# Performance work log

Hardware: AMD Instinct MI355X
Metric: run time of the kernel (lower is better)

## Reference

```python
import jax, jax.numpy as jnp
import numpy as np


def setup_inputs() -> dict:
    B, Lq, Lk, D, F, H = 2, 2048, 2048, 128, 128, 8
    key = jax.random.key(0)
    ks = jax.random.split(key, 8)
    X_Q = jax.random.normal(ks[0], (B, Lq, D), dtype=jnp.float32)
    X_K = jax.random.normal(ks[1], (B, Lk, D), dtype=jnp.float32)
    X_V = jax.random.normal(ks[2], (B, Lk, F), dtype=jnp.float32)
    mask = jax.random.randint(ks[3], (B, 1, Lq, Lk), 0, 2, dtype=jnp.int32)
    # xavier_normal for [H, D, D]: std = sqrt(2/(D+D))
    W_Q = jax.random.normal(ks[4], (H, D, D), dtype=jnp.float32) * np.sqrt(2.0 / (D + D))
    W_K = jax.random.normal(ks[5], (H, D, D), dtype=jnp.float32) * np.sqrt(2.0 / (D + D))
    W_V = jax.random.normal(ks[6], (H, F, F), dtype=jnp.float32) * np.sqrt(2.0 / (F + F))
    O = jax.random.normal(ks[7], (F * H, F), dtype=jnp.float32) * np.sqrt(2.0 / (F * H + F))
    return {"X_Q": X_Q, "X_K": X_K, "X_V": X_V, "mask": mask,
            "W_Q": W_Q, "W_K": W_K, "W_V": W_V, "O": O}


def reference(X_Q, X_K, X_V, mask, W_Q, W_K, W_V, O):
    B, Lq, D = X_Q.shape
    H = W_Q.shape[0]
    F = W_V.shape[1]
    # torch.einsum with repeated in-operand index ('hdd') takes the diagonal
    dq = jnp.diagonal(W_Q, axis1=1, axis2=2)  # [H, D]
    dk = jnp.diagonal(W_K, axis1=1, axis2=2)  # [H, D]
    dv = jnp.diagonal(W_V, axis1=1, axis2=2)  # [H, F]
    g = dq * dk                               # fused per-head QK diagonal scale [H, D]
    scale = 1.0 / jnp.sqrt(jnp.asarray(D, dtype=X_Q.dtype))
    scores = jnp.einsum('bqd,hd,bkd->bhqk', X_Q, g, X_K) * scale  # [B,H,Lq,Lk]
    scores = jnp.where(mask == 0, jnp.asarray(-jnp.inf, scores.dtype), scores)
    A = jax.nn.softmax(scores, axis=-1)
    # O_h = A @ (diag(dv_h) scaled V)
    Oh = jnp.einsum('bhqk,hf,bkf->bhqf', A, dv, X_V)  # [B,H,Lq,F]
    Oh = Oh.transpose(0, 2, 1, 3).reshape(B, Lq, H * F)
    return jnp.einsum('bqx,xf->bqf', Oh, O)
```

## Files before the change

kernel.cpp:

```cpp
#include <hip/hip_runtime.h>

typedef __bf16 bf16;
typedef __bf16 bf16x4 __attribute__((ext_vector_type(4)));
typedef __bf16 bf16x8 __attribute__((ext_vector_type(8)));
typedef float f32x4 __attribute__((ext_vector_type(4)));
typedef short s16x4 __attribute__((ext_vector_type(4)));
typedef unsigned int u32;
typedef unsigned long long u64;

#define B_ 2
#define H_ 8
#define L_ 2048
#define D_ 128
#define F_ 128
#define QT 128
#define KT 64
#define NKT (L_ / KT)

#define WS_KB 0u
#define WS_VT (1u << 20)
#define WS_MB (2u << 20)

#define SMEM_BYTES 102400
#define POX_STRIDE 132
#define SOH_OFF 67584
#define SOH_STRIDE 136
#define SO2_STRIDE 136

__device__ __forceinline__ void dma16(const void* g, void* l) {
    __builtin_amdgcn_global_load_lds(
        (const __attribute__((address_space(1))) u32*)g,
        (__attribute__((address_space(3))) u32*)l, 16, 0, 0);
}

__device__ __forceinline__ f32x4 mfma32(bf16x8 a, bf16x8 b, f32x4 c) {
    return __builtin_amdgcn_mfma_f32_16x16x32_bf16(a, b, c, 0, 0, 0);
}

__device__ __forceinline__ f32x4 mfma16(bf16x4 a, bf16x4 b, f32x4 c) {
#if __has_builtin(__builtin_amdgcn_mfma_f32_16x16x16_bf16)
    return __builtin_amdgcn_mfma_f32_16x16x16_bf16(a, b, c, 0, 0, 0);
#else
    s16x4 as = __builtin_bit_cast(s16x4, a);
    s16x4 bs = __builtin_bit_cast(s16x4, b);
    return __builtin_amdgcn_mfma_f32_16x16x16bf16_1k(as, bs, c, 0, 0, 0);
#endif
}

__device__ __forceinline__ float fexp2(float x) {
#if __has_builtin(__builtin_amdgcn_exp2f)
    return __builtin_amdgcn_exp2f(x);
#else
    return __builtin_exp2f(x);
#endif
}

__global__ __launch_bounds__(256)
void prep_all(const float* __restrict__ XK, const float* __restrict__ XV,
              const int* __restrict__ mask, bf16* __restrict__ Kb,
              bf16* __restrict__ Vtb, u64* __restrict__ bits)
{
    const int bid = blockIdx.x;
    const int tid = threadIdx.x;
    if (bid < 8192) {
        int wv = bid * 4 + (tid >> 6);
        int lane = tid & 63;
        size_t base = (size_t)wv * 256;
        #pragma unroll
        for (int s = 0; s < 4; ++s) {
            int m = mask[base + s * 64 + lane];
            u64 bal = __ballot(m != 0);
            if (lane == 0) bits[(size_t)wv * 4 + s] = bal;
        }
    } else if (bid < 8448) {
        int gid = (bid - 8192) * 256 + tid;
        int row = gid >> 4;
        int j   = gid & 15;
        const float* src = XK + (size_t)row * 128 + j * 8;
        float4 v0 = *(const float4*)src;
        float4 v1 = *(const float4*)(src + 4);
        bf16x8 w;
        w[0] = (bf16)v0.x; w[1] = (bf16)v0.y; w[2] = (bf16)v0.z; w[3] = (bf16)v0.w;
        w[4] = (bf16)v1.x; w[5] = (bf16)v1.y; w[6] = (bf16)v1.z; w[7] = (bf16)v1.w;
        int jp = j ^ (row & 15);
        *(bf16x8*)(Kb + (size_t)row * 128 + jp * 8) = w;
    } else {
        int idx  = bid - 8448;
        int tile = idx >> 2;
        int fq   = idx & 3;
        int f    = fq * 32 + (tid & 31);
        int j    = tid >> 5;
        int bb   = tile >> 5, kt = tile & 31;
        const float* src = XV + ((size_t)(bb * L_ + kt * 64 + j * 8)) * F_ + f;
        bf16x4 w0, w1;
        #pragma unroll
        for (int jj = 0; jj < 4; ++jj) {
            w0[jj] = (bf16)src[(size_t)jj * F_];
            w1[jj] = (bf16)src[(size_t)(4 + jj) * F_];
        }
        bf16* outp = Vtb + (size_t)tile * 8192 + f * 64;
        *(bf16x4*)(outp + (((2 * j) ^ (f & 15)) * 4)) = w0;
        *(bf16x4*)(outp + (((2 * j + 1) ^ (f & 15)) * 4)) = w1;
    }
}

__global__ __launch_bounds__(512, 2)
void attn_fused_kernel(const float* __restrict__ XQ, const bf16* __restrict__ Kb,
                       const bf16* __restrict__ Vtb, const u64* __restrict__ bits,
                       const float* __restrict__ WQ, const float* __restrict__ WK,
                       const float* __restrict__ WV, const float* __restrict__ Om,
                       float* __restrict__ out)
{
    __shared__ __align__(16) char smem[SMEM_BYTES];
    __shared__ __align__(16) float g_s[128];
    __shared__ __align__(16) float lws[256];

    bf16* sK0 = (bf16*)smem;
    bf16* sK1 = (bf16*)(smem + 16384);
    bf16* sV0 = (bf16*)(smem + 32768);
    bf16* sV1 = (bf16*)(smem + 49152);
    float* pOx = (float*)smem;
    bf16* sOh  = (bf16*)(smem + SOH_OFF);
    bf16* sO2t = (bf16*)smem;

    const int tid  = threadIdx.x;
    const int wave = tid >> 6;
    const int lane = tid & 63;
    const int c    = lane & 15;
    const int quad = lane >> 4;
    const int qt = blockIdx.x, h = blockIdx.y, b = blockIdx.z;
    const int q0 = qt * QT;

    const int kh   = wave >> 2;
    const int msel = wave & 3;
    const int fv  = tid & 127;
    const int grp = tid >> 7;

    if (tid < 128) {
        float wq = WQ[(h * D_ + tid) * D_ + tid];
        float wk = WK[(h * D_ + tid) * D_ + tid];
        g_s[tid] = wq * wk * 0.08838834764831845f * 1.4426950408889634f;
    }
    __syncthreads();

    const char* gKbase = (const char*)Kb + (size_t)(b * L_) * 256;
    const char* gVbase = (const char*)Vtb + (size_t)(b * NKT) * 16384;

    #pragma unroll
    for (int i = 0; i < 2; ++i) dma16(gKbase + i * 8192 + tid * 16, (char*)sK0 + i * 8192 + tid * 16);
    #pragma unroll
    for (int i = 0; i < 2; ++i) dma16(gVbase + i * 8192 + tid * 16, (char*)sV0 + i * 8192 + tid * 16);

    bf16x8 qfrag[2][4];
    #pragma unroll
    for (int qs = 0; qs < 2; ++qs) {
        const float* qrow = XQ + (size_t)(b * L_ + q0 + (qs * 4 + msel) * 16 + c) * D_;
        #pragma unroll
        for (int kc = 0; kc < 4; ++kc) {
            int d0 = kc * 32 + quad * 8;
            float4 v0 = *(const float4*)(qrow + d0);
            float4 v1 = *(const float4*)(qrow + d0 + 4);
            float4 g0 = *(const float4*)(g_s + d0);
            float4 g1 = *(const float4*)(g_s + d0 + 4);
            bf16x8 w;
            w[0] = (bf16)(v0.x * g0.x); w[1] = (bf16)(v0.y * g0.y);
            w[2] = (bf16)(v0.z * g0.z); w[3] = (bf16)(v0.w * g0.w);
            w[4] = (bf16)(v1.x * g1.x); w[5] = (bf16)(v1.y * g1.y);
            w[6] = (bf16)(v1.z * g1.z); w[7] = (bf16)(v1.w * g1.w);
            qfrag[qs][kc] = w;
        }
    }

    f32x4 oacc[2][8];
    #pragma unroll
    for (int qs = 0; qs < 2; ++qs)
        #pragma unroll
        for (int fi = 0; fi < 8; ++fi)
            #pragma unroll
            for (int r = 0; r < 4; ++r) oacc[qs][fi][r] = 0.f;
    float lsum0 = 0.f, lsum1 = 0.f;

    const u64* mrowA = bits + (size_t)(b * L_ + q0 + msel * 16 + c) * NKT;
    const u64* mrowB = bits + (size_t)(b * L_ + q0 + (msel + 4) * 16 + c) * NKT;

    #pragma unroll 2
    for (int kt = 0; kt < NKT; ++kt) {
        bf16* sK  = (kt & 1) ? sK1 : sK0;
        bf16* sV  = (kt & 1) ? sV1 : sV0;
        bf16* sKn = (kt & 1) ? sK0 : sK1;
        bf16* sVn = (kt & 1) ? sV0 : sV1;

        asm volatile("s_barrier" ::: "memory");

        u64 mb0 = mrowA[kt];
        u64 mb1 = mrowB[kt];

        if (kt + 1 < NKT) {
            const char* gk = gKbase + (size_t)(kt + 1) * 16384;
            const char* gv = gVbase + (size_t)(kt + 1) * 16384;
            #pragma unroll
            for (int i = 0; i < 2; ++i) dma16(gk + i * 8192 + tid * 16, (char*)sKn + i * 8192 + tid * 16);
            #pragma unroll
            for (int i = 0; i < 2; ++i) dma16(gv + i * 8192 + tid * 16, (char*)sVn + i * 8192 + tid * 16);
            asm volatile("s_waitcnt vmcnt(6)" ::: "memory");
        } else {
            asm volatile("s_waitcnt vmcnt(2)" ::: "memory");
        }
        asm volatile("s_barrier" ::: "memory");

        f32x4 tacc[2][2];
        #pragma unroll
        for (int qs = 0; qs < 2; ++qs)
            #pragma unroll
            for (int kti = 0; kti < 2; ++kti)
                #pragma unroll
                for (int r = 0; r < 4; ++r) tacc[qs][kti][r] = 0.f;

        #pragma unroll
        for (int kti = 0; kti < 2; ++kti) {
            const bf16* krow = sK + ((kh * 2 + kti) * 16 + c) * 128;
            #pragma unroll
            for (int kc = 0; kc < 4; ++kc) {
                bf16x8 kfrag = *(const bf16x8*)(krow + (((kc * 4 + quad) ^ c) * 8));
                tacc[0][kti] = mfma32(kfrag, qfrag[0][kc], tacc[0][kti]);
                tacc[1][kti] = mfma32(kfrag, qfrag[1][kc], tacc[1][kti]);
            }
        }

        bf16x4 pfrag[2][2];
        #pragma unroll
        for (int kti = 0; kti < 2; ++kti) {
            #pragma unroll
            for (int r = 0; r < 4; ++r) {
                int bit = kh * 32 + kti * 16 + quad * 4 + r;
                float p0 = ((mb0 >> bit) & 1ull) ? fexp2(tacc[0][kti][r]) : 0.f;
                float p1 = ((mb1 >> bit) & 1ull) ? fexp2(tacc[1][kti][r]) : 0.f;
                lsum0 += p0; lsum1 += p1;
                pfrag[0][kti][r] = (bf16)p0;
                pfrag[1][kti][r] = (bf16)p1;
            }
        }

        #pragma unroll
        for (int fi = 0; fi < 8; ++fi) {
            #pragma unroll
            for (int kti = 0; kti < 2; ++kti) {
                int g = kh * 8 + kti * 4 + quad;
                bf16x4 vfrag = *(const bf16x4*)(sV + (fi * 16 + c) * 64 + ((g ^ c) * 4));
                oacc[0][fi] = mfma16(pfrag[0][kti], vfrag, oacc[0][fi]);
                oacc[1][fi] = mfma16(pfrag[1][kti], vfrag, oacc[1][fi]);
            }
        }
    }

    {
        float v0 = lsum0;
        v0 += __shfl_xor(v0, 16); v0 += __shfl_xor(v0, 32);
        if (lane < 16) lws[kh * 128 + msel * 16 + lane] = v0;
        float v1 = lsum1;
        v1 += __shfl_xor(v1, 16); v1 += __shfl_xor(v1, 32);
        if (lane < 16) lws[kh * 128 + (msel + 4) * 16 + lane] = v1;
    }
    if (tid < 128)
        g_s[tid] = WV[(h * F_ + tid) * F_ + tid];
    __syncthreads();

    if (kh == 1) {
        #pragma unroll
        for (int qs = 0; qs < 2; ++qs)
            #pragma unroll
            for (int fi = 0; fi < 8; ++fi)
                #pragma unroll
                for (int r = 0; r < 4; ++r)
                    pOx[((qs * 4 + msel) * 16 + quad * 4 + r) * POX_STRIDE + fi * 16 + c] = oacc[qs][fi][r];
    }
    __syncthreads();

    if (kh == 0) {
        #pragma unroll
        for (int qs = 0; qs < 2; ++qs) {
            int mt = qs * 4 + msel;
            float linv[4];
            #pragma unroll
            for (int r = 0; r < 4; ++r) {
                int m16 = quad * 4 + r;
                linv[r] = 1.0f / (lws[mt * 16 + m16] + lws[128 + mt * 16 + m16]);
            }
            #pragma unroll
            for (int fi = 0; fi < 8; ++fi)
                #pragma unroll
                for (int r = 0; r < 4; ++r) {
                    int row = mt * 16 + quad * 4 + r;
                    float v = (oacc[qs][fi][r] + pOx[row * POX_STRIDE + fi * 16 + c]) * linv[r];
                    sOh[row * SOH_STRIDE + fi * 16 + c] = (bf16)v;
                }
        }
    }
    __syncthreads();

    #pragma unroll
    for (int i = 0; i < 8; ++i) {
        int fp4 = grp * 32 + i * 4;
        bf16x4 w;
        #pragma unroll
        for (int j = 0; j < 4; ++j) {
            int x = fp4 + j;
            w[j] = (bf16)(Om[(h * F_ + x) * F_ + fv] * g_s[x]);
        }
        *(bf16x4*)(sO2t + fv * SO2_STRIDE + fp4) = w;
    }
    __syncthreads();

    const int pm = wave;
    bf16x8 afr[4];
    const bf16* ohrow = sOh + (pm * 16 + c) * SOH_STRIDE;
    #pragma unroll
    for (int kc = 0; kc < 4; ++kc)
        afr[kc] = *(const bf16x8*)(ohrow + kc * 32 + quad * 8);

    #pragma unroll
    for (int nt = 0; nt < 8; ++nt) {
        f32x4 pacc;
        #pragma unroll
        for (int r = 0; r < 4; ++r) pacc[r] = 0.f;
        const bf16* orow = sO2t + (nt * 16 + c) * SO2_STRIDE;
        #pragma unroll
        for (int kc = 0; kc < 4; ++kc) {
            bf16x8 bfrag = *(const bf16x8*)(orow + kc * 32 + quad * 8);
            pacc = mfma32(afr[kc], bfrag, pacc);
        }
        #pragma unroll
        for (int r = 0; r < 4; ++r) {
            int qg = q0 + pm * 16 + quad * 4 + r;
            atomicAdd(out + ((size_t)(b * L_ + qg) * F_ + nt * 16 + c), pacc[r]);
        }
    }
}

extern "C" void kernel_launch(void* const* d_in, const int* in_sizes, int n_in,
                              void* d_out, int out_size, void* d_ws, size_t ws_size,
                              hipStream_t stream) {
    const float* XQ   = (const float*)d_in[0];
    const float* XK   = (const float*)d_in[1];
    const float* XV   = (const float*)d_in[2];
    const int*   mask = (const int*)d_in[3];
    const float* WQ   = (const float*)d_in[4];
    const float* WK   = (const float*)d_in[5];
    const float* WV   = (const float*)d_in[6];
    const float* Om   = (const float*)d_in[7];
    float* out = (float*)d_out;

    char* ws = (char*)d_ws;
    bf16* Kb   = (bf16*)(ws + WS_KB);
    bf16* Vtb  = (bf16*)(ws + WS_VT);
    u64*  bits = (u64*)(ws + WS_MB);

    prep_all<<<8704, 256, 0, stream>>>(XK, XV, mask, Kb, Vtb, bits);
    hipMemsetAsync(out, 0, (size_t)out_size * sizeof(float), stream);

    dim3 grid(L_ / QT, H_, B_);
    attn_fused_kernel<<<grid, 512, 0, stream>>>(XQ, Kb, Vtb, bits, WQ, WK, WV, Om, out);
}
```

Measured before the change: 170.5 us.

## Halve query tile, split keys across four wave groups, raise occupancy

Shrinks the query tile from 128 to 64 rows and splits each 64-key tile across four wave groups instead of two, so each wave does half the score/PV work per tile. Shared memory drops and launch bounds request 4 blocks per CU, doubling the grid and aiming for more resident waves to hide latency. The mask word for the next tile is prefetched alongside the DMA, and the cross-wave output reduction now runs in two swizzled passes over three partial buffers. In exchange, each block reloads the full K/V stream for half as many queries, doubling K/V traffic, and the epilogue needs more barriers and reduction work.

```diff
diff --git a/kernel.cpp b/kernel.cpp
--- a/kernel.cpp
+++ b/kernel.cpp
@@ -13,7 +13,7 @@
 #define L_ 2048
 #define D_ 128
 #define F_ 128
-#define QT 128
+#define QT 64
 #define KT 64
 #define NKT (L_ / KT)
 
@@ -21,9 +21,8 @@
 #define WS_VT (1u << 20)
 #define WS_MB (2u << 20)
 
-#define SMEM_BYTES 102400
-#define POX_STRIDE 132
-#define SOH_OFF 67584
+#define SMEM_BYTES 66560
+#define SOH_OFF 49152
 #define SOH_STRIDE 136
 #define SO2_STRIDE 136
 
@@ -104,7 +103,7 @@
     }
 }
 
-__global__ __launch_bounds__(512, 2)
+__global__ __launch_bounds__(512, 4)
 void attn_fused_kernel(const float* __restrict__ XQ, const bf16* __restrict__ Kb,
                        const bf16* __restrict__ Vtb, const u64* __restrict__ bits,
                        const float* __restrict__ WQ, const float* __restrict__ WK,
@@ -131,8 +130,8 @@
     const int qt = blockIdx.x, h = blockIdx.y, b = blockIdx.z;
     const int q0 = qt * QT;
 
-    const int kh   = wave >> 2;
-    const int msel = wave & 3;
+    const int kq = wave >> 1;
+    const int mp = wave & 1;
     const int fv  = tid & 127;
     const int grp = tid >> 7;
 
@@ -151,10 +150,15 @@
     #pragma unroll
     for (int i = 0; i < 2; ++i) dma16(gVbase + i * 8192 + tid * 16, (char*)sV0 + i * 8192 + tid * 16);
 
+    const u64* mrowA = bits + (size_t)(b * L_ + q0 + mp * 16 + c) * NKT;
+    const u64* mrowB = bits + (size_t)(b * L_ + q0 + (mp + 2) * 16 + c) * NKT;
+    u64 mb0c = mrowA[0];
+    u64 mb1c = mrowB[0];
+
     bf16x8 qfrag[2][4];
     #pragma unroll
     for (int qs = 0; qs < 2; ++qs) {
-        const float* qrow = XQ + (size_t)(b * L_ + q0 + (qs * 4 + msel) * 16 + c) * D_;
+        const float* qrow = XQ + (size_t)(b * L_ + q0 + (qs * 2 + mp) * 16 + c) * D_;
         #pragma unroll
         for (int kc = 0; kc < 4; ++kc) {
             int d0 = kc * 32 + quad * 8;
@@ -180,9 +184,6 @@
             for (int r = 0; r < 4; ++r) oacc[qs][fi][r] = 0.f;
     float lsum0 = 0.f, lsum1 = 0.f;
 
-    const u64* mrowA = bits + (size_t)(b * L_ + q0 + msel * 16 + c) * NKT;
-    const u64* mrowB = bits + (size_t)(b * L_ + q0 + (msel + 4) * 16 + c) * NKT;
-
     #pragma unroll 2
     for (int kt = 0; kt < NKT; ++kt) {
         bf16* sK  = (kt & 1) ? sK1 : sK0;
@@ -192,8 +193,8 @@
 
         asm volatile("s_barrier" ::: "memory");
 
-        u64 mb0 = mrowA[kt];
-        u64 mb1 = mrowB[kt];
+        u64 mb0 = mb0c;
+        u64 mb1 = mb1c;
 
         if (kt + 1 < NKT) {
             const char* gk = gKbase + (size_t)(kt + 1) * 16384;
@@ -202,53 +203,48 @@
             for (int i = 0; i < 2; ++i) dma16(gk + i * 8192 + tid * 16, (char*)sKn + i * 8192 + tid * 16);
             #pragma unroll
             for (int i = 0; i < 2; ++i) dma16(gv + i * 8192 + tid * 16, (char*)sVn + i * 8192 + tid * 16);
+            mb0c = mrowA[kt + 1];
+            mb1c = mrowB[kt + 1];
             asm volatile("s_waitcnt vmcnt(6)" ::: "memory");
         } else {
             asm volatile("s_waitcnt vmcnt(2)" ::: "memory");
         }
         asm volatile("s_barrier" ::: "memory");
 
-        f32x4 tacc[2][2];
+        f32x4 tacc[2];
         #pragma unroll
         for (int qs = 0; qs < 2; ++qs)
             #pragma unroll
-            for (int kti = 0; kti < 2; ++kti)
-                #pragma unroll
-                for (int r = 0; r < 4; ++r) tacc[qs][kti][r] = 0.f;
-
-        #pragma unroll
-        for (int kti = 0; kti < 2; ++kti) {
-            const bf16* krow = sK + ((kh * 2 + kti) * 16 + c) * 128;
+            for (int r = 0; r < 4; ++r) tacc[qs][r] = 0.f;
+
+        {
+            const bf16* krow = sK + (kq * 16 + c) * 128;
             #pragma unroll
             for (int kc = 0; kc < 4; ++kc) {
                 bf16x8 kfrag = *(const bf16x8*)(krow + (((kc * 4 + quad) ^ c) * 8));
-                tacc[0][kti] = mfma32(kfrag, qfrag[0][kc], tacc[0][kti]);
-                tacc[1][kti] = mfma32(kfrag, qfrag[1][kc], tacc[1][kti]);
+                tacc[0] = mfma32(kfrag, qfrag[0][kc], tacc[0]);
+                tacc[1] = mfma32(kfrag, qfrag[1][kc], tacc[1]);
             }
         }
 
-        bf16x4 pfrag[2][2];
-        #pragma unroll
-        for (int kti = 0; kti < 2; ++kti) {
-            #pragma unroll
-            for (int r = 0; r < 4; ++r) {
-                int bit = kh * 32 + kti * 16 + quad * 4 + r;
-                float p0 = ((mb0 >> bit) & 1ull) ? fexp2(tacc[0][kti][r]) : 0.f;
-                float p1 = ((mb1 >> bit) & 1ull) ? fexp2(tacc[1][kti][r]) : 0.f;
-                lsum0 += p0; lsum1 += p1;
-                pfrag[0][kti][r] = (bf16)p0;
-                pfrag[1][kti][r] = (bf16)p1;
-            }
-        }
-
-        #pragma unroll
-        for (int fi = 0; fi < 8; ++fi) {
-            #pragma unroll
-            for (int kti = 0; kti < 2; ++kti) {
-                int g = kh * 8 + kti * 4 + quad;
+        bf16x4 pfrag[2];
+        #pragma unroll
+        for (int r = 0; r < 4; ++r) {
+            int bit = kq * 16 + quad * 4 + r;
+            float p0 = ((mb0 >> bit) & 1ull) ? fexp2(tacc[0][r]) : 0.f;
+            float p1 = ((mb1 >> bit) & 1ull) ? fexp2(tacc[1][r]) : 0.f;
+            lsum0 += p0; lsum1 += p1;
+            pfrag[0][r] = (bf16)p0;
+            pfrag[1][r] = (bf16)p1;
+        }
+
+        {
+            int g = kq * 4 + quad;
+            #pragma unroll
+            for (int fi = 0; fi < 8; ++fi) {
                 bf16x4 vfrag = *(const bf16x4*)(sV + (fi * 16 + c) * 64 + ((g ^ c) * 4));
-                oacc[0][fi] = mfma16(pfrag[0][kti], vfrag, oacc[0][fi]);
-                oacc[1][fi] = mfma16(pfrag[1][kti], vfrag, oacc[1][fi]);
+                oacc[0][fi] = mfma16(pfrag[0], vfrag, oacc[0][fi]);
+                oacc[1][fi] = mfma16(pfrag[1], vfrag, oacc[1][fi]);
             }
         }
     }
@@ -256,47 +252,60 @@
     {
         float v0 = lsum0;
         v0 += __shfl_xor(v0, 16); v0 += __shfl_xor(v0, 32);
-        if (lane < 16) lws[kh * 128 + msel * 16 + lane] = v0;
+        if (lane < 16) lws[kq * 64 + mp * 16 + lane] = v0;
         float v1 = lsum1;
         v1 += __shfl_xor(v1, 16); v1 += __shfl_xor(v1, 32);
-        if (lane < 16) lws[kh * 128 + (msel + 4) * 16 + lane] = v1;
+        if (lane < 16) lws[kq * 64 + (mp + 2) * 16 + lane] = v1;
     }
     if (tid < 128)
         g_s[tid] = WV[(h * F_ + tid) * F_ + tid];
     __syncthreads();
 
-    if (kh == 1) {
+    float linv[2][4];
+    if (kq == 0) {
         #pragma unroll
         for (int qs = 0; qs < 2; ++qs)
             #pragma unroll
-            for (int fi = 0; fi < 8; ++fi)
+            for (int r = 0; r < 4; ++r) {
+                int row = (qs * 2 + mp) * 16 + quad * 4 + r;
+                linv[qs][r] = 1.0f /
+                    (lws[row] + lws[64 + row] + lws[128 + row] + lws[192 + row]);
+            }
+    }
+
+    #pragma unroll
+    for (int r2 = 0; r2 < 2; ++r2) {
+        if (kq != 0) {
+            float* dst = pOx + (kq - 1) * 4096;
+            #pragma unroll
+            for (int qs = 0; qs < 2; ++qs)
                 #pragma unroll
-                for (int r = 0; r < 4; ++r)
-                    pOx[((qs * 4 + msel) * 16 + quad * 4 + r) * POX_STRIDE + fi * 16 + c] = oacc[qs][fi][r];
-    }
-    __syncthreads();
-
-    if (kh == 0) {
-        #pragma unroll
-        for (int qs = 0; qs < 2; ++qs) {
-            int mt = qs * 4 + msel;
-            float linv[4];
-            #pragma unroll
-            for (int r = 0; r < 4; ++r) {
-                int m16 = quad * 4 + r;
-                linv[r] = 1.0f / (lws[mt * 16 + m16] + lws[128 + mt * 16 + m16]);
-            }
-            #pragma unroll
-            for (int fi = 0; fi < 8; ++fi)
+                for (int fl = 0; fl < 4; ++fl)
+                    #pragma unroll
+                    for (int r = 0; r < 4; ++r) {
+                        int row = (qs * 2 + mp) * 16 + quad * 4 + r;
+                        int col = (fl * 16 + c) ^ (quad << 4);
+                        dst[row * 64 + col] = oacc[qs][r2 * 4 + fl][r];
+                    }
+        }
+        __syncthreads();
+        if (kq == 0) {
+            #pragma unroll
+            for (int qs = 0; qs < 2; ++qs)
                 #pragma unroll
-                for (int r = 0; r < 4; ++r) {
-                    int row = mt * 16 + quad * 4 + r;
-                    float v = (oacc[qs][fi][r] + pOx[row * POX_STRIDE + fi * 16 + c]) * linv[r];
-                    sOh[row * SOH_STRIDE + fi * 16 + c] = (bf16)v;
-                }
-        }
-    }
-    __syncthreads();
+                for (int fl = 0; fl < 4; ++fl)
+                    #pragma unroll
+                    for (int r = 0; r < 4; ++r) {
+                        int fi = r2 * 4 + fl;
+                        int row = (qs * 2 + mp) * 16 + quad * 4 + r;
+                        int col = (fl * 16 + c) ^ (quad << 4);
+                        float v = oacc[qs][fi][r] + pOx[row * 64 + col]
+                                + pOx[4096 + row * 64 + col] + pOx[8192 + row * 64 + col];
+                        sOh[row * SOH_STRIDE + fi * 16 + c] = (bf16)(v * linv[qs][r]);
+                    }
+        }
+        __syncthreads();
+    }
 
     #pragma unroll
     for (int i = 0; i < 8; ++i) {
@@ -311,7 +320,8 @@
     }
     __syncthreads();
 
-    const int pm = wave;
+    const int pm = wave & 3;
+    const int pf = wave >> 2;
     bf16x8 afr[4];
     const bf16* ohrow = sOh + (pm * 16 + c) * SOH_STRIDE;
     #pragma unroll
@@ -319,11 +329,11 @@
         afr[kc] = *(const bf16x8*)(ohrow + kc * 32 + quad * 8);
 
     #pragma unroll
-    for (int nt = 0; nt < 8; ++nt) {
+    for (int nt = 0; nt < 4; ++nt) {
         f32x4 pacc;
         #pragma unroll
         for (int r = 0; r < 4; ++r) pacc[r] = 0.f;
-        const bf16* orow = sO2t + (nt * 16 + c) * SO2_STRIDE;
+        const bf16* orow = sO2t + ((pf * 4 + nt) * 16 + c) * SO2_STRIDE;
         #pragma unroll
         for (int kc = 0; kc < 4; ++kc) {
             bf16x8 bfrag = *(const bf16x8*)(orow + kc * 32 + quad * 8);
@@ -332,7 +342,7 @@
         #pragma unroll
         for (int r = 0; r < 4; ++r) {
             int qg = q0 + pm * 16 + quad * 4 + r;
-            atomicAdd(out + ((size_t)(b * L_ + qg) * F_ + nt * 16 + c), pacc[r]);
+            atomicAdd(out + ((size_t)(b * L_ + qg) * F_ + (pf * 4 + nt) * 16 + c), pacc[r]);
         }
     }
 }
```

New measurement: 527.9 us. 3.1x slower.

## Halve query tile to 64 rows, doubling grid and cutting LDS and registers

Applied to the files above, without the earlier changes.

The query tile shrinks from 128 to 64 rows, so each wave handles one 16-row M-tile instead of two. This halves accumulator registers and LDS use, and the grid doubles to 512 blocks, which should improve occupancy and load balance across CUs. The change also prefetches mask words one iteration ahead with adjusted waitcnt, raises wave priority during the MFMA section, and splits the output projection across waves by N. In exchange, each K/V tile is reused by half as many queries, so global K/V traffic per output doubles.

```diff
diff --git a/kernel.cpp b/kernel.cpp
--- a/kernel.cpp
+++ b/kernel.cpp
@@ -13,7 +13,7 @@
 #define L_ 2048
 #define D_ 128
 #define F_ 128
-#define QT 128
+#define QT 64
 #define KT 64
 #define NKT (L_ / KT)
 
@@ -21,9 +21,10 @@
 #define WS_VT (1u << 20)
 #define WS_MB (2u << 20)
 
-#define SMEM_BYTES 102400
+#define SMEM_BYTES 66048
+#define LWS_OFF 65536
 #define POX_STRIDE 132
-#define SOH_OFF 67584
+#define SOH_OFF 36864
 #define SOH_STRIDE 136
 #define SO2_STRIDE 136
 
@@ -104,7 +105,7 @@
     }
 }
 
-__global__ __launch_bounds__(512, 2)
+__global__ __launch_bounds__(512)
 void attn_fused_kernel(const float* __restrict__ XQ, const bf16* __restrict__ Kb,
                        const bf16* __restrict__ Vtb, const u64* __restrict__ bits,
                        const float* __restrict__ WQ, const float* __restrict__ WK,
@@ -113,12 +114,12 @@
 {
     __shared__ __align__(16) char smem[SMEM_BYTES];
     __shared__ __align__(16) float g_s[128];
-    __shared__ __align__(16) float lws[256];
 
     bf16* sK0 = (bf16*)smem;
     bf16* sK1 = (bf16*)(smem + 16384);
     bf16* sV0 = (bf16*)(smem + 32768);
     bf16* sV1 = (bf16*)(smem + 49152);
+    float* lws = (float*)(smem + LWS_OFF);
     float* pOx = (float*)smem;
     bf16* sOh  = (bf16*)(smem + SOH_OFF);
     bf16* sO2t = (bf16*)smem;
@@ -151,10 +152,12 @@
     #pragma unroll
     for (int i = 0; i < 2; ++i) dma16(gVbase + i * 8192 + tid * 16, (char*)sV0 + i * 8192 + tid * 16);
 
-    bf16x8 qfrag[2][4];
-    #pragma unroll
-    for (int qs = 0; qs < 2; ++qs) {
-        const float* qrow = XQ + (size_t)(b * L_ + q0 + (qs * 4 + msel) * 16 + c) * D_;
+    const u64* mrow = bits + (size_t)(b * L_ + q0 + msel * 16 + c) * NKT;
+    u64 mbc = mrow[0];
+
+    bf16x8 qfrag[4];
+    {
+        const float* qrow = XQ + (size_t)(b * L_ + q0 + msel * 16 + c) * D_;
         #pragma unroll
         for (int kc = 0; kc < 4; ++kc) {
             int d0 = kc * 32 + quad * 8;
@@ -167,21 +170,16 @@
             w[2] = (bf16)(v0.z * g0.z); w[3] = (bf16)(v0.w * g0.w);
             w[4] = (bf16)(v1.x * g1.x); w[5] = (bf16)(v1.y * g1.y);
             w[6] = (bf16)(v1.z * g1.z); w[7] = (bf16)(v1.w * g1.w);
-            qfrag[qs][kc] = w;
-        }
-    }
-
-    f32x4 oacc[2][8];
-    #pragma unroll
-    for (int qs = 0; qs < 2; ++qs)
-        #pragma unroll
-        for (int fi = 0; fi < 8; ++fi)
-            #pragma unroll
-            for (int r = 0; r < 4; ++r) oacc[qs][fi][r] = 0.f;
-    float lsum0 = 0.f, lsum1 = 0.f;
-
-    const u64* mrowA = bits + (size_t)(b * L_ + q0 + msel * 16 + c) * NKT;
-    const u64* mrowB = bits + (size_t)(b * L_ + q0 + (msel + 4) * 16 + c) * NKT;
+            qfrag[kc] = w;
+        }
+    }
+
+    f32x4 oacc[8];
+    #pragma unroll
+    for (int fi = 0; fi < 8; ++fi)
+        #pragma unroll
+        for (int r = 0; r < 4; ++r) oacc[fi][r] = 0.f;
+    float lsum = 0.f;
 
     #pragma unroll 2
     for (int kt = 0; kt < NKT; ++kt) {
@@ -192,8 +190,7 @@
 
         asm volatile("s_barrier" ::: "memory");
 
-        u64 mb0 = mrowA[kt];
-        u64 mb1 = mrowB[kt];
+        u64 mb = mbc;
 
         if (kt + 1 < NKT) {
             const char* gk = gKbase + (size_t)(kt + 1) * 16384;
@@ -202,19 +199,20 @@
             for (int i = 0; i < 2; ++i) dma16(gk + i * 8192 + tid * 16, (char*)sKn + i * 8192 + tid * 16);
             #pragma unroll
             for (int i = 0; i < 2; ++i) dma16(gv + i * 8192 + tid * 16, (char*)sVn + i * 8192 + tid * 16);
-            asm volatile("s_waitcnt vmcnt(6)" ::: "memory");
+            mbc = mrow[kt + 1];
+            asm volatile("s_waitcnt vmcnt(5)" ::: "memory");
         } else {
-            asm volatile("s_waitcnt vmcnt(2)" ::: "memory");
+            asm volatile("s_waitcnt vmcnt(0)" ::: "memory");
         }
         asm volatile("s_barrier" ::: "memory");
 
-        f32x4 tacc[2][2];
-        #pragma unroll
-        for (int qs = 0; qs < 2; ++qs)
-            #pragma unroll
-            for (int kti = 0; kti < 2; ++kti)
-                #pragma unroll
-                for (int r = 0; r < 4; ++r) tacc[qs][kti][r] = 0.f;
+        __builtin_amdgcn_s_setprio(1);
+
+        f32x4 tacc[2];
+        #pragma unroll
+        for (int kti = 0; kti < 2; ++kti)
+            #pragma unroll
+            for (int r = 0; r < 4; ++r) tacc[kti][r] = 0.f;
 
         #pragma unroll
         for (int kti = 0; kti < 2; ++kti) {
@@ -222,22 +220,19 @@
             #pragma unroll
             for (int kc = 0; kc < 4; ++kc) {
                 bf16x8 kfrag = *(const bf16x8*)(krow + (((kc * 4 + quad) ^ c) * 8));
-                tacc[0][kti] = mfma32(kfrag, qfrag[0][kc], tacc[0][kti]);
-                tacc[1][kti] = mfma32(kfrag, qfrag[1][kc], tacc[1][kti]);
+                tacc[kti] = mfma32(kfrag, qfrag[kc], tacc[kti]);
             }
         }
 
-        bf16x4 pfrag[2][2];
+        bf16x4 pfrag[2];
         #pragma unroll
         for (int kti = 0; kti < 2; ++kti) {
             #pragma unroll
             for (int r = 0; r < 4; ++r) {
-                int bit = kh * 32 + kti * 16 + quad * 4 + r;
-                float p0 = ((mb0 >> bit) & 1ull) ? fexp2(tacc[0][kti][r]) : 0.f;
-                float p1 = ((mb1 >> bit) & 1ull) ? fexp2(tacc[1][kti][r]) : 0.f;
-                lsum0 += p0; lsum1 += p1;
-                pfrag[0][kti][r] = (bf16)p0;
-                pfrag[1][kti][r] = (bf16)p1;
+                float p = ((mb >> (kh * 32 + kti * 16 + quad * 4 + r)) & 1ull)
+                          ? fexp2(tacc[kti][r]) : 0.f;
+                lsum += p;
+                pfrag[kti][r] = (bf16)p;
             }
         }
 
@@ -247,19 +242,17 @@
             for (int kti = 0; kti < 2; ++kti) {
                 int g = kh * 8 + kti * 4 + quad;
                 bf16x4 vfrag = *(const bf16x4*)(sV + (fi * 16 + c) * 64 + ((g ^ c) * 4));
-                oacc[0][fi] = mfma16(pfrag[0][kti], vfrag, oacc[0][fi]);
-                oacc[1][fi] = mfma16(pfrag[1][kti], vfrag, oacc[1][fi]);
+                oacc[fi] = mfma16(pfrag[kti], vfrag, oacc[fi]);
             }
         }
+
+        __builtin_amdgcn_s_setprio(0);
     }
 
     {
-        float v0 = lsum0;
-        v0 += __shfl_xor(v0, 16); v0 += __shfl_xor(v0, 32);
-        if (lane < 16) lws[kh * 128 + msel * 16 + lane] = v0;
-        float v1 = lsum1;
-        v1 += __shfl_xor(v1, 16); v1 += __shfl_xor(v1, 32);
-        if (lane < 16) lws[kh * 128 + (msel + 4) * 16 + lane] = v1;
+        float v = lsum;
+        v += __shfl_xor(v, 16); v += __shfl_xor(v, 32);
+        if (lane < 16) lws[wave * 16 + lane] = v;
     }
     if (tid < 128)
         g_s[tid] = WV[(h * F_ + tid) * F_ + tid];
@@ -267,34 +260,28 @@
 
     if (kh == 1) {
         #pragma unroll
-        for (int qs = 0; qs < 2; ++qs)
-            #pragma unroll
-            for (int fi = 0; fi < 8; ++fi)
-                #pragma unroll
-                for (int r = 0; r < 4; ++r)
-                    pOx[((qs * 4 + msel) * 16 + quad * 4 + r) * POX_STRIDE + fi * 16 + c] = oacc[qs][fi][r];
+        for (int fi = 0; fi < 8; ++fi)
+            #pragma unroll
+            for (int r = 0; r < 4; ++r)
+                pOx[(msel * 16 + quad * 4 + r) * POX_STRIDE + fi * 16 + c] = oacc[fi][r];
     }
     __syncthreads();
 
     if (kh == 0) {
-        #pragma unroll
-        for (int qs = 0; qs < 2; ++qs) {
-            int mt = qs * 4 + msel;
-            float linv[4];
+        float linv[4];
+        #pragma unroll
+        for (int r = 0; r < 4; ++r) {
+            int m16 = quad * 4 + r;
+            linv[r] = 1.0f / (lws[msel * 16 + m16] + lws[(4 + msel) * 16 + m16]);
+        }
+        #pragma unroll
+        for (int fi = 0; fi < 8; ++fi)
             #pragma unroll
             for (int r = 0; r < 4; ++r) {
-                int m16 = quad * 4 + r;
-                linv[r] = 1.0f / (lws[mt * 16 + m16] + lws[128 + mt * 16 + m16]);
+                int row = msel * 16 + quad * 4 + r;
+                float v = (oacc[fi][r] + pOx[row * POX_STRIDE + fi * 16 + c]) * linv[r];
+                sOh[row * SOH_STRIDE + fi * 16 + c] = (bf16)v;
             }
-            #pragma unroll
-            for (int fi = 0; fi < 8; ++fi)
-                #pragma unroll
-                for (int r = 0; r < 4; ++r) {
-                    int row = mt * 16 + quad * 4 + r;
-                    float v = (oacc[qs][fi][r] + pOx[row * POX_STRIDE + fi * 16 + c]) * linv[r];
-                    sOh[row * SOH_STRIDE + fi * 16 + c] = (bf16)v;
-                }
-        }
     }
     __syncthreads();
 
@@ -311,7 +298,8 @@
     }
     __syncthreads();
 
-    const int pm = wave;
+    const int pm = wave & 3;
+    const int pf = wave >> 2;
     bf16x8 afr[4];
     const bf16* ohrow = sOh + (pm * 16 + c) * SOH_STRIDE;
     #pragma unroll
@@ -319,11 +307,11 @@
         afr[kc] = *(const bf16x8*)(ohrow + kc * 32 + quad * 8);
 
     #pragma unroll
-    for (int nt = 0; nt < 8; ++nt) {
+    for (int nt = 0; nt < 4; ++nt) {
         f32x4 pacc;
         #pragma unroll
         for (int r = 0; r < 4; ++r) pacc[r] = 0.f;
-        const bf16* orow = sO2t + (nt * 16 + c) * SO2_STRIDE;
+        const bf16* orow = sO2t + ((pf * 4 + nt) * 16 + c) * SO2_STRIDE;
         #pragma unroll
         for (int kc = 0; kc < 4; ++kc) {
             bf16x8 bfrag = *(const bf16x8*)(orow + kc * 32 + quad * 8);
@@ -332,7 +320,7 @@
         #pragma unroll
         for (int r = 0; r < 4; ++r) {
             int qg = q0 + pm * 16 + quad * 4 + r;
-            atomicAdd(out + ((size_t)(b * L_ + qg) * F_ + nt * 16 + c), pacc[r]);
+            atomicAdd(out + ((size_t)(b * L_ + qg) * F_ + (pf * 4 + nt) * 16 + c), pacc[r]);
         }
     }
 }
```

Result: faster. 156.3 us (-8.3%).
